# Optimization experiments

Measured on AMD Instinct MI355X. Metric: run time of the kernel, lower is better.

Reference implementation:

```python
import jax, jax.numpy as jnp
import numpy as np

S = 4096          # number of samples
N_NODES = 2048    # sum nodes in this layer
N_CHILD = 4096    # nodes per child layer
NNZ = 32768       # nonzeros per sparse log-weight matrix


def setup_inputs() -> dict:
    key = jax.random.key(0)
    ks = jax.random.split(key, 8)
    ll0 = jax.random.normal(ks[0], (S, N_CHILD), dtype=jnp.float32)
    ll1 = jax.random.normal(ks[1], (S, N_CHILD), dtype=jnp.float32)
    w0_data = jax.random.normal(ks[2], (NNZ,), dtype=jnp.float32)
    w1_data = jax.random.normal(ks[3], (NNZ,), dtype=jnp.float32)
    w0_rows = jax.random.randint(ks[4], (NNZ,), 0, N_NODES, dtype=jnp.int32)
    w0_cols = jax.random.randint(ks[5], (NNZ,), 0, N_CHILD, dtype=jnp.int32)
    w1_rows = jax.random.randint(ks[6], (NNZ,), 0, N_NODES, dtype=jnp.int32)
    w1_cols = jax.random.randint(ks[7], (NNZ,), 0, N_CHILD, dtype=jnp.int32)
    return {"ll0": ll0, "ll1": ll1,
            "w0_data": w0_data, "w1_data": w1_data,
            "w0_rows": w0_rows, "w0_cols": w0_cols,
            "w1_rows": w1_rows, "w1_cols": w1_cols,
            "n_nodes": N_NODES}


def _sparse_weighted_sum(ll, data, rows, cols, n_nodes):
    # exp(ll) @ exp(W).T for BCOO W with shape (n_nodes, n_child)
    # contrib[s, k] = exp(ll[s, cols[k]]) * exp(data[k]); scatter-add over rows.
    contrib = jnp.exp(ll[:, cols] + data[None, :])  # (S, NNZ)
    return jnp.zeros((ll.shape[0], n_nodes), dtype=ll.dtype).at[:, rows].add(contrib)


def reference(ll0, ll1, w0_data, w1_data, w0_rows, w0_cols, w1_rows, w1_cols, n_nodes):
    # accumulate exp(ll_i) @ exp(W_i).T over child layers
    result = _sparse_weighted_sum(ll0, w0_data, w0_rows, w0_cols, n_nodes)
    result = result + _sparse_weighted_sum(ll1, w1_data, w1_rows, w1_cols, n_nodes)
    # log normalization constants: log(sum_j exp(concatenated log_weights)[i, j])
    z = jnp.zeros((n_nodes,), dtype=result.dtype)
    z = z.at[w0_rows].add(jnp.exp(w0_data))
    z = z.at[w1_rows].add(jnp.exp(w1_data))
    return jnp.log(result) - jnp.log(z)[None, :]
```

## Files before the change

kernel.cpp:

```cpp
#include <hip/hip_runtime.h>
#include <math.h>

#define S 4096
#define N_NODES 2048
#define N_CHILD 4096
#define NNZ 32768
#define NNZ_TOTAL (2 * NNZ)
#define TSM 512
#define TN 8
#define CAP 96
#define LP 516

typedef float f32x2 __attribute__((ext_vector_type(2)));


__global__ __launch_bounds__(1024, 8) void prep_kernel(
        const float* __restrict__ ll0, const float* __restrict__ ll1,
        const float* __restrict__ w0d, const float* __restrict__ w1d,
        const int* __restrict__ w0r, const int* __restrict__ w0c,
        const int* __restrict__ w1r, const int* __restrict__ w1c,
        unsigned char* __restrict__ ET, int2* __restrict__ ent,
        int* __restrict__ counts) {
    __shared__ unsigned short tile[64 * 130];
    int t = threadIdx.x;
    int b = blockIdx.x;
    if (b < 64) {
        int k = b * 1024 + t;
        int row, col; float w;
        if (k < NNZ) { row = w0r[k]; col = w0c[k]; w = w0d[k]; }
        else { int kk = k - NNZ; row = w1r[kk]; col = w1c[kk] + N_CHILD; w = w1d[kk]; }
        int pos = atomicAdd(&counts[row], 1);
        if (pos < CAP)
            ent[row * CAP + pos] = make_int2(col, __float_as_int(__expf(w)));
        return;
    }
    int bt = b - 64;
    int slice = bt & 7;
    int sthalf = (bt >> 3) & 1;
    int ct = (bt >> 4) & 63;
    int z = (bt >> 10) & 1;
    int c0 = ct * 64;
    int s0 = slice * 512 + sthalf * 256;
    const float* ll = z ? ll1 : ll0;
    int wave = t >> 6, lane = t & 63;
    float v0[8], v1[8];
    const float* p = ll + (size_t)(s0 + wave * 2) * N_CHILD + c0 + lane;
#pragma unroll
    for (int it = 0; it < 8; ++it) {
        v0[it] = p[0];
        v1[it] = p[N_CHILD];
        p += 32 * (size_t)N_CHILD;
    }
    __builtin_amdgcn_sched_barrier(0);
#pragma unroll
    for (int it = 0; it < 8; ++it) {
        int sh = it * 16 + wave;
        unsigned int packed = (unsigned int)__builtin_amdgcn_cvt_pk_fp8_f32(
            __expf(v0[it]), __expf(v1[it]), 0, false);
        tile[lane * 130 + sh] = (unsigned short)packed;
    }
    __syncthreads();
    unsigned char* dst = ET + (size_t)(z * N_CHILD + c0) * S + s0;
#pragma unroll
    for (int it = 0; it < 4; ++it) {
        int c = it * 16 + wave;
        unsigned int v = *(const unsigned int*)&tile[c * 130 + lane * 2];
        *(unsigned int*)(dst + (size_t)c * S + lane * 4) = v;
    }
}


static __device__ inline void fma16(uint4 x, float w, float* a) {
#pragma unroll
    for (int q = 0; q < 4; ++q) {
        unsigned int word = (q == 0) ? x.x : (q == 1) ? x.y : (q == 2) ? x.z : x.w;
        f32x2 lo = __builtin_amdgcn_cvt_pk_f32_fp8(word, false);
        f32x2 hi = __builtin_amdgcn_cvt_pk_f32_fp8(word, true);
        a[q * 4 + 0] = fmaf(lo.x, w, a[q * 4 + 0]);
        a[q * 4 + 1] = fmaf(lo.y, w, a[q * 4 + 1]);
        a[q * 4 + 2] = fmaf(hi.x, w, a[q * 4 + 2]);
        a[q * 4 + 3] = fmaf(hi.y, w, a[q * 4 + 3]);
    }
}

static __device__ inline void entry_get(int t2, int hs, int cnt, int2 eA, int2 eB,
                                        int& col, float& w) {
    int k = hs + 2 * t2;
    int c, wi;
    if (t2 < 32) { c = __shfl(eA.x, k); wi = __shfl(eA.y, k); }
    else         { c = __shfl(eB.x, k - 64); wi = __shfl(eB.y, k - 64); }
    col = c & (2 * N_CHILD - 1);
    w = (k < cnt) ? __uint_as_float(wi) : 0.f;
}

__global__ __launch_bounds__(256, 4) void main_kernel(
        const unsigned char* __restrict__ ET, const int2* __restrict__ ent,
        const int* __restrict__ counts, float* __restrict__ out) {
    __shared__ float lds[TN * LP];
    int t = threadIdx.x, wave = t >> 6, lane = t & 63;
    int hs = lane >> 5, sl = lane & 31;
    int slice = blockIdx.x & 7;
    int nb = blockIdx.x >> 3;
    int i0 = nb * TN;
    const unsigned char* ETs = ET + slice * TSM + sl * 16;
    for (int jj = 0; jj < 2; ++jj) {
        int j = wave * 2 + jj;
        int i = i0 + j;
        int cnt = __builtin_amdgcn_readfirstlane(counts[i]);
        if (cnt > CAP) cnt = CAP;
        const int2* eb = ent + i * CAP;
        int2 eA = eb[lane];
        int2 eB = eb[64 + (lane & 31)];
        float a[16];
#pragma unroll
        for (int u = 0; u < 16; ++u) a[u] = 0.f;
        float z = 0.f;
        int nmax = (cnt + 1) >> 1;
        int t2 = 0;
        for (; t2 + 3 < nmax; t2 += 4) {
            int c0i, c1i, c2i, c3i; float w0, w1, w2, w3;
            entry_get(t2 + 0, hs, cnt, eA, eB, c0i, w0);
            entry_get(t2 + 1, hs, cnt, eA, eB, c1i, w1);
            entry_get(t2 + 2, hs, cnt, eA, eB, c2i, w2);
            entry_get(t2 + 3, hs, cnt, eA, eB, c3i, w3);
            uint4 x0 = *(const uint4*)(ETs + (size_t)c0i * S);
            uint4 x1 = *(const uint4*)(ETs + (size_t)c1i * S);
            uint4 x2 = *(const uint4*)(ETs + (size_t)c2i * S);
            uint4 x3 = *(const uint4*)(ETs + (size_t)c3i * S);
            fma16(x0, w0, a); fma16(x1, w1, a);
            fma16(x2, w2, a); fma16(x3, w3, a);
            z += w0 + w1 + w2 + w3;
        }
        for (; t2 < nmax; ++t2) {
            int c0i; float w0;
            entry_get(t2, hs, cnt, eA, eB, c0i, w0);
            uint4 x0 = *(const uint4*)(ETs + (size_t)c0i * S);
            fma16(x0, w0, a);
            z += w0;
        }
#pragma unroll
        for (int u = 0; u < 16; ++u) a[u] += __shfl_xor(a[u], 32);
        z += __shfl_xor(z, 32);
        float lz = __logf(z);
        float r[8];
#pragma unroll
        for (int u = 0; u < 8; ++u) r[u] = __logf(a[hs * 8 + u]) - lz;
        float* dstl = &lds[j * LP + sl * 16 + hs * 8];
        *(float4*)(dstl)     = make_float4(r[0], r[1], r[2], r[3]);
        *(float4*)(dstl + 4) = make_float4(r[4], r[5], r[6], r[7]);
    }
    __syncthreads();
    float* obase = out + (size_t)slice * TSM * N_NODES + i0;
#pragma unroll
    for (int q = 0; q < 8; ++q) {
        int elem = (t + 256 * q) * 2;
        int s_l = elem >> 3;
        int i_l = elem & 7;
        f32x2 v;
        v.x = lds[i_l * LP + s_l];
        v.y = lds[(i_l + 1) * LP + s_l];
        __builtin_nontemporal_store(v, (f32x2*)&obase[(size_t)s_l * N_NODES + i_l]);
    }
}


extern "C" void kernel_launch(void* const* d_in, const int* in_sizes, int n_in,
                              void* d_out, int out_size, void* d_ws, size_t ws_size,
                              hipStream_t stream) {
    const float* ll0 = (const float*)d_in[0];
    const float* ll1 = (const float*)d_in[1];
    const float* w0d = (const float*)d_in[2];
    const float* w1d = (const float*)d_in[3];
    const int*   w0r = (const int*)d_in[4];
    const int*   w0c = (const int*)d_in[5];
    const int*   w1r = (const int*)d_in[6];
    const int*   w1c = (const int*)d_in[7];
    float* out = (float*)d_out;

    unsigned char* ET = (unsigned char*)d_ws;
    int2* ent   = (int2*)(ET + (size_t)2 * N_CHILD * S);
    int*  counts = (int*)(ent + (size_t)N_NODES * CAP);

    hipMemsetAsync(counts, 0, sizeof(int) * N_NODES, stream);
    prep_kernel<<<2112, 1024, 0, stream>>>(ll0, ll1, w0d, w1d, w0r, w0c, w1r, w1c,
                                           ET, ent, counts);
    main_kernel<<<(N_NODES / TN) * (S / TSM), 256, 0, stream>>>(ET, ent, counts, out);
}
```

Measured before the change: 229.4 us.

## Use float4 loads and byte LDS tile in prep transpose; unroll gather by 8

Measured after the change: 237.0 us. +3.3%, slower.

```diff
diff --git a/kernel.cpp b/kernel.cpp
--- a/kernel.cpp
+++ b/kernel.cpp
@@ -10,22 +10,23 @@
 #define TN 8
 #define CAP 96
 #define LP 516
+#define TP 132
 
 typedef float f32x2 __attribute__((ext_vector_type(2)));
 
 
-__global__ __launch_bounds__(1024, 8) void prep_kernel(
+__global__ __launch_bounds__(512, 4) void prep_kernel(
         const float* __restrict__ ll0, const float* __restrict__ ll1,
         const float* __restrict__ w0d, const float* __restrict__ w1d,
         const int* __restrict__ w0r, const int* __restrict__ w0c,
         const int* __restrict__ w1r, const int* __restrict__ w1c,
         unsigned char* __restrict__ ET, int2* __restrict__ ent,
         int* __restrict__ counts) {
-    __shared__ unsigned short tile[64 * 130];
+    __shared__ unsigned char tile[128 * TP];
     int t = threadIdx.x;
     int b = blockIdx.x;
-    if (b < 64) {
-        int k = b * 1024 + t;
+    if (b < 128) {
+        int k = b * 512 + t;
         int row, col; float w;
         if (k < NNZ) { row = w0r[k]; col = w0c[k]; w = w0d[k]; }
         else { int kk = k - NNZ; row = w1r[kk]; col = w1c[kk] + N_CHILD; w = w1d[kk]; }
@@ -34,38 +35,39 @@
             ent[row * CAP + pos] = make_int2(col, __float_as_int(__expf(w)));
         return;
     }
-    int bt = b - 64;
+    int bt = b - 128;
     int slice = bt & 7;
-    int sthalf = (bt >> 3) & 1;
-    int ct = (bt >> 4) & 63;
+    int sq = (bt >> 3) & 3;
+    int ct = (bt >> 5) & 31;
     int z = (bt >> 10) & 1;
-    int c0 = ct * 64;
-    int s0 = slice * 512 + sthalf * 256;
+    int c0 = ct * 128;
+    int s0 = slice * 512 + sq * 128;
     const float* ll = z ? ll1 : ll0;
     int wave = t >> 6, lane = t & 63;
-    float v0[8], v1[8];
-    const float* p = ll + (size_t)(s0 + wave * 2) * N_CHILD + c0 + lane;
+    int colg = (lane & 31) * 4;
+    int rbase = wave * 2 + (lane >> 5);
+    float4 v[8];
+    const float* p = ll + (size_t)(s0 + rbase) * N_CHILD + c0 + colg;
 #pragma unroll
-    for (int it = 0; it < 8; ++it) {
-        v0[it] = p[0];
-        v1[it] = p[N_CHILD];
-        p += 32 * (size_t)N_CHILD;
-    }
+    for (int st = 0; st < 8; ++st)
+        v[st] = *(const float4*)(p + (size_t)st * 16 * N_CHILD);
     __builtin_amdgcn_sched_barrier(0);
 #pragma unroll
-    for (int it = 0; it < 8; ++it) {
-        int sh = it * 16 + wave;
-        unsigned int packed = (unsigned int)__builtin_amdgcn_cvt_pk_fp8_f32(
-            __expf(v0[it]), __expf(v1[it]), 0, false);
-        tile[lane * 130 + sh] = (unsigned short)packed;
+    for (int st = 0; st < 8; ++st) {
+        int r = st * 16 + rbase;
+        unsigned char* d = &tile[colg * TP + r];
+        d[0 * TP] = (unsigned char)__builtin_amdgcn_cvt_pk_fp8_f32(__expf(v[st].x), 0.f, 0, false);
+        d[1 * TP] = (unsigned char)__builtin_amdgcn_cvt_pk_fp8_f32(__expf(v[st].y), 0.f, 0, false);
+        d[2 * TP] = (unsigned char)__builtin_amdgcn_cvt_pk_fp8_f32(__expf(v[st].z), 0.f, 0, false);
+        d[3 * TP] = (unsigned char)__builtin_amdgcn_cvt_pk_fp8_f32(__expf(v[st].w), 0.f, 0, false);
     }
     __syncthreads();
     unsigned char* dst = ET + (size_t)(z * N_CHILD + c0) * S + s0;
 #pragma unroll
-    for (int it = 0; it < 4; ++it) {
-        int c = it * 16 + wave;
-        unsigned int v = *(const unsigned int*)&tile[c * 130 + lane * 2];
-        *(unsigned int*)(dst + (size_t)c * S + lane * 4) = v;
+    for (int st = 0; st < 8; ++st) {
+        int c = st * 16 + wave * 2 + (lane >> 5);
+        unsigned int w = *(const unsigned int*)&tile[c * TP + 4 * (lane & 31)];
+        *(unsigned int*)(dst + (size_t)c * S + 4 * (lane & 31)) = w;
     }
 }
 
@@ -117,19 +119,25 @@
         float z = 0.f;
         int nmax = (cnt + 1) >> 1;
         int t2 = 0;
+        for (; t2 + 7 < nmax; t2 += 8) {
+            int c[8]; float w[8];
+#pragma unroll
+            for (int u = 0; u < 8; ++u) entry_get(t2 + u, hs, cnt, eA, eB, c[u], w[u]);
+            uint4 x[8];
+#pragma unroll
+            for (int u = 0; u < 8; ++u) x[u] = *(const uint4*)(ETs + (size_t)c[u] * S);
+#pragma unroll
+            for (int u = 0; u < 8; ++u) { fma16(x[u], w[u], a); z += w[u]; }
+        }
         for (; t2 + 3 < nmax; t2 += 4) {
-            int c0i, c1i, c2i, c3i; float w0, w1, w2, w3;
-            entry_get(t2 + 0, hs, cnt, eA, eB, c0i, w0);
-            entry_get(t2 + 1, hs, cnt, eA, eB, c1i, w1);
-            entry_get(t2 + 2, hs, cnt, eA, eB, c2i, w2);
-            entry_get(t2 + 3, hs, cnt, eA, eB, c3i, w3);
-            uint4 x0 = *(const uint4*)(ETs + (size_t)c0i * S);
-            uint4 x1 = *(const uint4*)(ETs + (size_t)c1i * S);
-            uint4 x2 = *(const uint4*)(ETs + (size_t)c2i * S);
-            uint4 x3 = *(const uint4*)(ETs + (size_t)c3i * S);
-            fma16(x0, w0, a); fma16(x1, w1, a);
-            fma16(x2, w2, a); fma16(x3, w3, a);
-            z += w0 + w1 + w2 + w3;
+            int c[4]; float w[4];
+#pragma unroll
+            for (int u = 0; u < 4; ++u) entry_get(t2 + u, hs, cnt, eA, eB, c[u], w[u]);
+            uint4 x[4];
+#pragma unroll
+            for (int u = 0; u < 4; ++u) x[u] = *(const uint4*)(ETs + (size_t)c[u] * S);
+#pragma unroll
+            for (int u = 0; u < 4; ++u) { fma16(x[u], w[u], a); z += w[u]; }
         }
         for (; t2 < nmax; ++t2) {
             int c0i; float w0;
@@ -182,7 +190,7 @@
     int*  counts = (int*)(ent + (size_t)N_NODES * CAP);
 
     hipMemsetAsync(counts, 0, sizeof(int) * N_NODES, stream);
-    prep_kernel<<<2112, 1024, 0, stream>>>(ll0, ll1, w0d, w1d, w0r, w0c, w1r, w1c,
-                                           ET, ent, counts);
+    prep_kernel<<<2176, 512, 0, stream>>>(ll0, ll1, w0d, w1d, w0r, w0c, w1r, w1c,
+                                          ET, ent, counts);
     main_kernel<<<(N_NODES / TN) * (S / TSM), 256, 0, stream>>>(ET, ent, counts, out);
 }
```
